# Kernel tuning notes

Hardware: AMD Instinct MI355X
Metric: run time of the kernel (lower is better)

## Reference

```python
import jax, jax.numpy as jnp
import numpy as np

H = 8
D_MODEL = 1024
D_K = D_MODEL // H
NEG = -1000000000.0


def layer_norm(x, a, b, eps=1e-06):
    # torch std: unbiased (ddof=1); module divides by (std + eps)
    mean = jnp.mean(x, axis=-1, keepdims=True)
    var = jnp.sum((x - mean) ** 2, axis=-1, keepdims=True) / (x.shape[-1] - 1)
    std = jnp.sqrt(var)
    return a * (x - mean) / (std + eps) + b


def setup_inputs() -> dict:
    key = jax.random.key(0)
    ks = jax.random.split(key, 12)
    B, S, D = 8, 1024, D_MODEL
    inp = {
        "query": jax.random.normal(ks[0], (B, S, D), jnp.float32),
        "value": jax.random.normal(ks[1], (B, S, D), jnp.float32),
        "key": jax.random.normal(ks[2], (B, S, D), jnp.float32),
        "mask": jax.random.randint(ks[3], (B, S), 0, 2, jnp.int32),
        "ln_a": jnp.ones((D,), jnp.float32),
        "ln_b": jnp.zeros((D,), jnp.float32),
        "wq": jax.random.normal(ks[4], (D, D), jnp.float32) * 0.02,
        "bq": jnp.zeros((D,), jnp.float32),
        "wk": jax.random.normal(ks[5], (D, D), jnp.float32) * 0.02,
        "bk": jnp.zeros((D,), jnp.float32),
        "wv": jax.random.normal(ks[6], (D, D), jnp.float32) * 0.02,
        "bv": jnp.zeros((D,), jnp.float32),
        "w_aoa": jax.random.normal(ks[7], (2 * D, 2 * D), jnp.float32) * 0.02,  # [out, in]
        "b_aoa": jnp.zeros((2 * D,), jnp.float32),
    }
    return inp


def reference(query, value, key, mask, ln_a, ln_b, wq, bq, wk, bk, wv, bv, w_aoa, b_aoa):
    B, S, D = query.shape
    # mask [B,S] -> [B,1,1,S]
    m = mask[:, None, None, :]
    # norm_q
    q = layer_norm(query, ln_a, ln_b)
    # QKV projections, split heads -> [B,H,S,Dk]
    def split_heads(x):
        return x.reshape(B, -1, H, D_K).transpose(0, 2, 1, 3)
    q_ = split_heads(q @ wq.T + bq)
    k_ = split_heads(key @ wk.T + bk)
    v_ = split_heads(value @ wv.T + bv)
    scores = jnp.einsum("bhqd,bhkd->bhqk", q_, k_) / jnp.sqrt(jnp.float32(D_K))
    scores = jnp.where(m == 0, NEG, scores)
    p = jax.nn.softmax(scores, axis=-1)
    x = jnp.einsum("bhqk,bhkd->bhqd", p, v_)
    x = x.transpose(0, 2, 1, 3).reshape(B, S, D)
    # AoA: concat with (normed) query, linear to 2D, GLU
    z = jnp.concatenate([x, q], axis=-1) @ w_aoa.T + b_aoa
    a, g = jnp.split(z, 2, axis=-1)
    return a * jax.nn.sigmoid(g)
```

## Files before the change

kernel.cpp:

```cpp
#include <hip/hip_runtime.h>

typedef __attribute__((ext_vector_type(8))) __bf16 bf16x8;
typedef __attribute__((ext_vector_type(4))) float f32x4;

__device__ __forceinline__ ushort f2b(float f) {
    uint u = __builtin_bit_cast(uint, f);
    u += 0x7fffu + ((u >> 16) & 1u);
    return (ushort)(u >> 16);
}
__device__ __forceinline__ float b2f(ushort h) {
    uint u = ((uint)h) << 16;
    return __builtin_bit_cast(float, u);
}

__global__ __launch_bounds__(256) void cast_kernel(const float* __restrict__ src,
                                                   ushort* __restrict__ dst) {
    size_t i = ((size_t)blockIdx.x * 256 + threadIdx.x) * 4;
    float4 v = *(const float4*)(src + i);
    ushort4 o;
    o.x = f2b(v.x); o.y = f2b(v.y); o.z = f2b(v.z); o.w = f2b(v.w);
    *(ushort4*)(dst + i) = o;
}

__global__ __launch_bounds__(256) void cast_permute_aoa(const float* __restrict__ src,
                                                        ushort* __restrict__ dst) {
    int n1 = blockIdx.x >> 1;
    int c = (blockIdx.x & 1) * 1024 + threadIdx.x * 4;
    int q = ((n1 & 63) | ((n1 >> 7) << 6)) + ((n1 >> 6) & 1) * 1024;
    float4 v = *(const float4*)(src + (size_t)q * 2048 + c);
    ushort4 o;
    o.x = f2b(v.x); o.y = f2b(v.y); o.z = f2b(v.z); o.w = f2b(v.w);
    *(ushort4*)(dst + (size_t)n1 * 2048 + c) = o;
}

__global__ __launch_bounds__(256) void ln_kernel(const float* __restrict__ x,
                                                 const float* __restrict__ ga,
                                                 const float* __restrict__ be,
                                                 ushort* __restrict__ xq) {
    const int row = blockIdx.x, tid = threadIdx.x;
    __shared__ float red[4];
    float4 v = ((const float4*)(x + (size_t)row * 1024))[tid];
    float sm = v.x + v.y + v.z + v.w;
    for (int off = 32; off; off >>= 1) sm += __shfl_xor(sm, off);
    if ((tid & 63) == 0) red[tid >> 6] = sm;
    __syncthreads();
    float mean = (red[0] + red[1] + red[2] + red[3]) * (1.f / 1024.f);
    __syncthreads();
    float dx = v.x - mean, dy = v.y - mean, dz = v.z - mean, dw = v.w - mean;
    float s2 = dx * dx + dy * dy + dz * dz + dw * dw;
    for (int off = 32; off; off >>= 1) s2 += __shfl_xor(s2, off);
    if ((tid & 63) == 0) red[tid >> 6] = s2;
    __syncthreads();
    float var = (red[0] + red[1] + red[2] + red[3]) * (1.f / 1023.f);
    float inv = 1.f / (sqrtf(var) + 1e-6f);
    float4 g = ((const float4*)ga)[tid];
    float4 bb = ((const float4*)be)[tid];
    ushort4 o;
    o.x = f2b(g.x * dx * inv + bb.x);
    o.y = f2b(g.y * dy * inv + bb.y);
    o.z = f2b(g.z * dz * inv + bb.z);
    o.w = f2b(g.w * dw * inv + bb.w);
    *(ushort4*)&xq[(size_t)row * 2048 + 1024 + tid * 4] = o;
}

template <int MODE>
__global__ __launch_bounds__(512, 2) void gemm5(const ushort* __restrict__ Aq, int ldaq,
                                                const ushort* __restrict__ Ak,
                                                const ushort* __restrict__ Av,
                                                const ushort* __restrict__ B, int ldb,
                                                const float* __restrict__ bias0,
                                                const float* __restrict__ bias1,
                                                const float* __restrict__ bias2,
                                                void* __restrict__ out0,
                                                void* __restrict__ out1,
                                                void* __restrict__ out2,
                                                int K, int NB, float qscale) {
    __shared__ ushort lds[2][32768];

    const int tid = threadIdx.x;
    const int w = tid >> 6, l = tid & 63;
    const int wr = w >> 2, wcn = w & 3;
    const int r16 = l & 15, g4 = l >> 4;

    const int bid = blockIdx.x;
    const int cpx = gridDim.x >> 3;
    const int swz = (bid & 7) * cpx + (bid >> 3);
    const int m0 = (swz / NB) * 256;
    const int n0 = (swz % NB) * 256;

    const int region = (MODE == 0) ? (n0 >> 10) : 0;
    const ushort* A = (MODE == 0) ? (region == 0 ? Aq : (region == 1 ? Ak : Av)) : Aq;
    const int lda = (MODE == 0) ? (region == 0 ? ldaq : 1024) : ldaq;

    const int srow8 = l >> 3;
    const int sxor8 = ((l & 7) ^ srow8) * 8;
    const ushort* As0 = A + (size_t)(m0 + w * 8 + srow8) * lda + sxor8;
    const ushort* Bs0 = B + (size_t)(n0 + w * 8 + srow8) * ldb + sxor8;

    f32x4 acc[8][4];
#pragma unroll
    for (int i = 0; i < 8; i++)
#pragma unroll
        for (int j = 0; j < 4; j++) acc[i][j] = (f32x4){0.f, 0.f, 0.f, 0.f};

    const int sw16 = (r16 & 7) << 4;
    char* ldsb = (char*)&lds[0][0];

#define STAGE_H(sel_, HS_, kt_)                                                            \
    do {                                                                                   \
        const int mat_ = (HS_)&1, half_ = (HS_) >> 1;                                      \
        const ushort* sb_ = mat_ ? Bs0 : As0;                                              \
        const int ld_ = mat_ ? ldb : lda;                                                  \
        _Pragma("unroll") for (int li_ = 0; li_ < 2; li_++) {                              \
            const ushort* src_ = sb_ + (size_t)(half_ * 128 + li_ * 64) * ld_ + (kt_)*64;  \
            int dst_ = (sel_)*65536 + mat_ * 32768 + half_ * 16384 + li_ * 8192 + w * 1024;\
            __builtin_amdgcn_global_load_lds(                                              \
                (const __attribute__((address_space(1))) void*)src_,                       \
                (__attribute__((address_space(3))) void*)(ldsb + dst_), 16, 0, 0);         \
        }                                                                                  \
    } while (0)

    auto LDA4 = [&](bf16x8 (&dst)[4][2], int sel, int half) {
#pragma unroll
        for (int ai = 0; ai < 4; ai++)
#pragma unroll
            for (int ks = 0; ks < 2; ks++)
                dst[ai][ks] = *(const bf16x8*)(ldsb + sel * 65536 + half * 16384 +
                                               (wr * 16 + 32 * ai + r16) * 128 +
                                               ((ks * 64 + g4 * 16) ^ sw16));
    };
    auto LDB2 = [&](bf16x8 (&dst)[2][2], int sel, int half) {
#pragma unroll
        for (int bi = 0; bi < 2; bi++)
#pragma unroll
            for (int ks = 0; ks < 2; ks++)
                dst[bi][ks] = *(const bf16x8*)(ldsb + sel * 65536 + 32768 + half * 16384 +
                                               (wcn * 16 + 64 * bi + r16) * 128 +
                                               ((ks * 64 + g4 * 16) ^ sw16));
    };
    auto MM = [&](bf16x8 (&af)[4][2], bf16x8 (&bf)[2][2], int A0, int B0) {
        __builtin_amdgcn_s_setprio(1);
#pragma unroll
        for (int ks = 0; ks < 2; ks++)
#pragma unroll
            for (int ai = 0; ai < 4; ai++)
#pragma unroll
                for (int bi = 0; bi < 2; bi++)
                    acc[A0 + ai][B0 + bi] = __builtin_amdgcn_mfma_f32_16x16x32_bf16(
                        af[ai][ks], bf[bi][ks], acc[A0 + ai][B0 + bi], 0, 0, 0);
        __builtin_amdgcn_s_setprio(0);
    };

    const int NT = K >> 6;

    STAGE_H(0, 0, 0); STAGE_H(0, 1, 0); STAGE_H(0, 2, 0); STAGE_H(0, 3, 0);
    asm volatile("s_waitcnt vmcnt(0)" ::: "memory");
    __builtin_amdgcn_s_barrier();

    bf16x8 aL[4][2], aH[4][2], bL[2][2], bH[2][2];

    for (int t = 0; t < NT; ++t) {
        const int sel = t & 1;
        const bool pf = (t + 1 < NT);
        LDA4(aL, sel, 0); LDB2(bL, sel, 0);
        if (pf) STAGE_H(sel ^ 1, 0, t + 1);
        __builtin_amdgcn_s_barrier();
        MM(aL, bL, 0, 0);
        asm volatile("s_waitcnt vmcnt(4)" ::: "memory");
        __builtin_amdgcn_s_barrier();
        LDA4(aH, sel, 1);
        if (pf) STAGE_H(sel ^ 1, 1, t + 1);
        __builtin_amdgcn_s_barrier();
        MM(aH, bL, 4, 0);
        asm volatile("s_waitcnt vmcnt(4)" ::: "memory");
        __builtin_amdgcn_s_barrier();
        LDB2(bH, sel, 1);
        if (pf) STAGE_H(sel ^ 1, 2, t + 1);
        __builtin_amdgcn_s_barrier();
        MM(aH, bH, 4, 2);
        asm volatile("s_waitcnt vmcnt(4)" ::: "memory");
        __builtin_amdgcn_s_barrier();
        if (pf) STAGE_H(sel ^ 1, 3, t + 1);
        __builtin_amdgcn_s_barrier();
        MM(aL, bH, 0, 2);
        asm volatile("s_waitcnt vmcnt(4)" ::: "memory");
        __builtin_amdgcn_s_barrier();
    }
#undef STAGE_H

    if (MODE == 1) {
        float* out = (float*)out0;
#pragma unroll
        for (int bp = 0; bp < 2; bp++) {
            int j = (n0 >> 1) + wcn * 16 + 64 * bp + r16;
            float bsa = bias0[j];
            float bsg = bias0[j + 1024];
#pragma unroll
            for (int a_ = 0; a_ < 8; a_++) {
                int mr = m0 + wr * 16 + 32 * a_ + g4 * 4;
#pragma unroll
                for (int r = 0; r < 4; r++) {
                    float av = acc[a_][2 * bp][r] + bsa;
                    float gv = acc[a_][2 * bp + 1][r] + bsg;
                    out[(size_t)(mr + r) * 1024 + j] = av * (1.f / (1.f + __expf(-gv)));
                }
            }
        }
    } else {
        const int nr0 = n0 & 1023;
        const float* bias = region == 0 ? bias0 : (region == 1 ? bias1 : bias2);
        const float scale = region == 0 ? qscale : 1.f;
        if (region < 2) {
            ushort* C = (ushort*)(region == 0 ? out0 : out1);
#pragma unroll
            for (int b_ = 0; b_ < 4; b_++) {
                int n = nr0 + wcn * 16 + 64 * b_ + r16;
                float bs = bias[n];
#pragma unroll
                for (int a_ = 0; a_ < 8; a_++) {
                    int mr = m0 + wr * 16 + 32 * a_ + g4 * 4;
#pragma unroll
                    for (int r = 0; r < 4; r++)
                        C[(size_t)(mr + r) * 1024 + n] = f2b((acc[a_][b_][r] + bs) * scale);
                }
            }
        } else {
            ushort* Vt = (ushort*)out2;
#pragma unroll
            for (int b_ = 0; b_ < 4; b_++) {
                int n = nr0 + wcn * 16 + 64 * b_ + r16;
                float bs = bias[n];
                int h = n >> 7, d = n & 127;
#pragma unroll
                for (int a_ = 0; a_ < 8; a_++) {
                    int mr = m0 + wr * 16 + 32 * a_ + g4 * 4;
                    int bb = mr >> 10, s_ = mr & 1023;
                    ushort4 o;
                    o.x = f2b(acc[a_][b_][0] + bs);
                    o.y = f2b(acc[a_][b_][1] + bs);
                    o.z = f2b(acc[a_][b_][2] + bs);
                    o.w = f2b(acc[a_][b_][3] + bs);
                    *(ushort4*)&Vt[((size_t)(bb * 8 + h) * 128 + d) * 1024 + s_] = o;
                }
            }
        }
    }
}

__global__ __launch_bounds__(512, 4) void attn_kernel(const ushort* __restrict__ Q,
                                                      const ushort* __restrict__ Kt,
                                                      const ushort* __restrict__ Vt,
                                                      const int* __restrict__ mask,
                                                      ushort* __restrict__ xq) {
    __shared__ ushort Ks[2][8192];
    __shared__ ushort Vs[2][8192];
    __shared__ ushort Pl[8][1024];

    const int tid = threadIdx.x;
    const int l = tid & 63, wid = tid >> 6;
    const int r16 = l & 15, g4 = l >> 4;
    const int id = blockIdx.x;
    const int bh = ((id >> 6) << 3) | (id & 7);
    const int qb = (id >> 3) & 7;
    const int b = bh >> 3, h = bh & 7;
    const int q0 = qb * 128 + wid * 16;

    bf16x8 qf[4];
    const ushort* Qrow = Q + (size_t)(b * 1024 + q0 + r16) * 1024 + h * 128 + g4 * 8;
#pragma unroll
    for (int kf = 0; kf < 4; kf++) qf[kf] = *(const bf16x8*)(Qrow + kf * 32);

    const ushort* Kg = Kt + ((size_t)b * 1024) * 1024 + h * 128;
    const ushort* Vg = Vt + (size_t)(b * 8 + h) * 128 * 1024;
    const int* mptr = mask + b * 1024;

    f32x4 xacc[8];
#pragma unroll
    for (int i = 0; i < 8; i++) xacc[i] = (f32x4){0.f, 0.f, 0.f, 0.f};
    float mrow = -INFINITY, lrow = 0.f, sclp = 0.f;

    char* Pme = (char*)&Pl[wid][0];
    const int pswz = (r16 & 7) << 4;

    auto STAGE_K = [&](int sel, int t) {
        const int kv0 = t * 64;
#pragma unroll
        for (int it = 0; it < 2; ++it) {
            int ob = it * 8192 + wid * 1024;
            int o = ob + l * 16;
            int row = o >> 8;
            int sc = (o & 255) ^ ((row & 7) << 4);
            const ushort* src = Kg + (size_t)(kv0 + row) * 1024 + (sc >> 1);
            __builtin_amdgcn_global_load_lds((const __attribute__((address_space(1))) void*)src,
                (__attribute__((address_space(3))) void*)((char*)&Ks[sel][0] + ob), 16, 0, 0);
        }
    };
    auto STAGE_V = [&](int sel, int t) {
        const int kv0 = t * 64;
#pragma unroll
        for (int it = 0; it < 2; ++it) {
            int ob = it * 8192 + wid * 1024;
            int o = ob + l * 16;
            int d = o >> 7;
            int sc = (o & 127) ^ ((d & 7) << 4);
            const ushort* src = Vg + (size_t)d * 1024 + kv0 + (sc >> 1);
            __builtin_amdgcn_global_load_lds((const __attribute__((address_space(1))) void*)src,
                (__attribute__((address_space(3))) void*)((char*)&Vs[sel][0] + ob), 16, 0, 0);
        }
    };

    auto QK = [&](f32x4 (&s)[4], int sel, unsigned long long wt) {
        const char* Kb_ = (const char*)&Ks[sel][0];
#pragma unroll
        for (int cg = 0; cg < 4; cg++) {
            s[cg] = (f32x4){0.f, 0.f, 0.f, 0.f};
            const int rowk = cg * 16 + r16;
            const char* kr = Kb_ + rowk * 256;
            const int sw = (rowk & 7) << 4;
            __builtin_amdgcn_s_setprio(1);
#pragma unroll
            for (int kf = 0; kf < 4; kf++) {
                bf16x8 kfr = *(const bf16x8*)(kr + ((kf * 64 + g4 * 16) ^ sw));
                s[cg] = __builtin_amdgcn_mfma_f32_16x16x32_bf16(kfr, qf[kf], s[cg], 0, 0, 0);
            }
            __builtin_amdgcn_s_setprio(0);
            uint nib = (uint)(wt >> (cg * 16 + g4 * 4)) & 15u;
#pragma unroll
            for (int r = 0; r < 4; r++)
                if (!((nib >> r) & 1u)) s[cg][r] = -1e9f;
        }
    };
    auto PV = [&](int sel) {
        const char* Vb_ = (const char*)&Vs[sel][0];
        bf16x8 pfr[2];
#pragma unroll
        for (int ks = 0; ks < 2; ks++)
            pfr[ks] = *(const bf16x8*)(Pme + r16 * 128 + ((g4 * 16 + ks * 64) ^ pswz));
#pragma unroll
        for (int cg2 = 0; cg2 < 8; cg2++)
#pragma unroll
            for (int r = 0; r < 4; r++) xacc[cg2][r] *= sclp;
        __builtin_amdgcn_s_setprio(1);
#pragma unroll
        for (int ks = 0; ks < 2; ks++) {
#pragma unroll
            for (int cg2 = 0; cg2 < 8; cg2++) {
                const int d = cg2 * 16 + r16;
                bf16x8 vfr = *(const bf16x8*)(Vb_ + d * 128 + ((ks * 64 + g4 * 16) ^ ((d & 7) << 4)));
                xacc[cg2] = __builtin_amdgcn_mfma_f32_16x16x32_bf16(vfr, pfr[ks], xacc[cg2], 0, 0, 0);
            }
        }
        __builtin_amdgcn_s_setprio(0);
    };
    auto SOFTMAX = [&](f32x4 (&s)[4]) {
        float pmax = -INFINITY;
#pragma unroll
        for (int cg = 0; cg < 4; cg++)
#pragma unroll
            for (int r = 0; r < 4; r++) pmax = fmaxf(pmax, s[cg][r]);
        pmax = fmaxf(pmax, __shfl_xor(pmax, 16));
        pmax = fmaxf(pmax, __shfl_xor(pmax, 32));
        float mn = fmaxf(mrow, pmax);
        sclp = __expf(mrow - mn);
        mrow = mn;
        float rsum = 0.f;
#pragma unroll
        for (int cg = 0; cg < 4; cg++)
#pragma unroll
            for (int r = 0; r < 4; r++) {
                float p = __expf(s[cg][r] - mn);
                s[cg][r] = p;
                rsum += p;
            }
        rsum += __shfl_xor(rsum, 16);
        rsum += __shfl_xor(rsum, 32);
        lrow = lrow * sclp + rsum;
#pragma unroll
        for (int cg = 0; cg < 4; cg++) {
            uint lo = ((uint)f2b(s[cg][1]) << 16) | f2b(s[cg][0]);
            uint hi = ((uint)f2b(s[cg][3]) << 16) | f2b(s[cg][2]);
            uint2 pk; pk.x = lo; pk.y = hi;
            *(uint2*)(Pme + r16 * 128 + ((cg * 32 + g4 * 8) ^ pswz)) = pk;
        }
    };

    STAGE_K(0, 0);
    int mv = mptr[l];
    asm volatile("s_waitcnt vmcnt(0)" ::: "memory");
    __syncthreads();
    STAGE_K(1, 1);
    STAGE_V(0, 0);
    unsigned long long wt = __ballot(mv != 0);
    mv = mptr[64 + l];
    {
        f32x4 s0[4];
        QK(s0, 0, wt);
        SOFTMAX(s0);
    }
    int kc = 1, vc = 0;

    for (int u = 1; u < 16; ++u) {
        wt = __ballot(mv != 0);
        asm volatile("s_waitcnt vmcnt(0)" ::: "memory");
        __syncthreads();
        if (u < 15) STAGE_K(kc ^ 1, u + 1);
        STAGE_V(vc ^ 1, u);
        if (u < 15) mv = mptr[(u + 1) * 64 + l];

        f32x4 sn[4];
        QK(sn, kc, wt);
        PV(vc);
        SOFTMAX(sn);

        kc ^= 1; vc ^= 1;
    }

    asm volatile("s_waitcnt vmcnt(0)" ::: "memory");
    __syncthreads();
    PV(vc);

    const float inv = 1.f / lrow;
    const size_t orow = (size_t)(b * 1024 + q0 + r16) * 2048 + h * 128;
#pragma unroll
    for (int cg2 = 0; cg2 < 8; cg2++) {
#pragma unroll
        for (int r = 0; r < 4; r++) {
            xq[orow + cg2 * 16 + g4 * 4 + r] = f2b(xacc[cg2][r] * inv);
        }
    }
}

extern "C" void kernel_launch(void* const* d_in, const int* in_sizes, int n_in,
                              void* d_out, int out_size, void* d_ws, size_t ws_size,
                              hipStream_t stream) {
    const float* query = (const float*)d_in[0];
    const float* value = (const float*)d_in[1];
    const float* key   = (const float*)d_in[2];
    const int*   mask  = (const int*)d_in[3];
    const float* ln_a  = (const float*)d_in[4];
    const float* ln_b  = (const float*)d_in[5];
    const float* wq    = (const float*)d_in[6];
    const float* bq    = (const float*)d_in[7];
    const float* wk    = (const float*)d_in[8];
    const float* bk    = (const float*)d_in[9];
    const float* wv    = (const float*)d_in[10];
    const float* bv    = (const float*)d_in[11];
    const float* waoa  = (const float*)d_in[12];
    const float* baoa  = (const float*)d_in[13];
    float* out = (float*)d_out;

    char* w8 = (char*)d_ws;
    ushort* xq   = (ushort*)(w8);
    ushort* Qb   = (ushort*)(w8 + 33554432);
    ushort* Kb   = (ushort*)(w8 + 50331648);
    ushort* Vt   = (ushort*)(w8 + 67108864);
    ushort* keyb = (ushort*)(w8 + 83886080);
    ushort* valb = (ushort*)(w8 + 100663296);
    ushort* wqb  = (ushort*)(w8 + 117440512);
    ushort* wkb  = (ushort*)(w8 + 119537664);
    ushort* wvb  = (ushort*)(w8 + 121634816);
    ushort* wab  = (ushort*)(w8 + 123731968);

    cast_kernel<<<8192, 256, 0, stream>>>(key, keyb);
    cast_kernel<<<8192, 256, 0, stream>>>(value, valb);
    cast_kernel<<<1024, 256, 0, stream>>>(wq, wqb);
    cast_kernel<<<1024, 256, 0, stream>>>(wk, wkb);
    cast_kernel<<<1024, 256, 0, stream>>>(wv, wvb);
    cast_permute_aoa<<<4096, 256, 0, stream>>>(waoa, wab);
    ln_kernel<<<8192, 256, 0, stream>>>(query, ln_a, ln_b, xq);

    const float qscale = 0.08838834764831845f;

    gemm5<0><<<384, 512, 0, stream>>>(xq + 1024, 2048, keyb, valb,
                                      wqb, 1024, bq, bk, bv,
                                      Qb, Kb, Vt, 1024, 12, qscale);

    attn_kernel<<<512, 512, 0, stream>>>(Qb, Kb, Vt, mask, xq);

    gemm5<1><<<256, 512, 0, stream>>>(xq, 2048, nullptr, nullptr,
                                      wab, 2048, baoa, nullptr, nullptr,
                                      out, nullptr, nullptr, 2048, 8, 1.f);
}
```

Measured before the change: 243.7 us.

## Deepen GEMM global-load prefetch to stage tiles two iterations ahead

Restructures the GEMM main loop so global-to-LDS staging runs further ahead. Most of tile t+1 is issued in the prologue, and within each iteration quarters of tile t+2 are staged into the buffer currently being read. The loop ends with two peeled epilogue iterations that drain outstanding loads using adjusted vmcnt waits. The aim is to hide more global memory latency behind MFMA work. It relies on careful barrier placement to avoid overwriting LDS data still being read, and it assumes NT >= 2.

```diff
diff --git a/kernel.cpp b/kernel.cpp
--- a/kernel.cpp
+++ b/kernel.cpp
@@ -64,7 +64,7 @@
 }
 
 template <int MODE>
-__global__ __launch_bounds__(512, 2) void gemm5(const ushort* __restrict__ Aq, int ldaq,
+__global__ __launch_bounds__(512, 2) void gemm6(const ushort* __restrict__ Aq, int ldaq,
                                                 const ushort* __restrict__ Ak,
                                                 const ushort* __restrict__ Av,
                                                 const ushort* __restrict__ B, int ldb,
@@ -154,37 +154,73 @@
     const int NT = K >> 6;
 
     STAGE_H(0, 0, 0); STAGE_H(0, 1, 0); STAGE_H(0, 2, 0); STAGE_H(0, 3, 0);
-    asm volatile("s_waitcnt vmcnt(0)" ::: "memory");
+    STAGE_H(1, 0, 1); STAGE_H(1, 1, 1); STAGE_H(1, 2, 1);
+    asm volatile("s_waitcnt vmcnt(10)" ::: "memory");
     __builtin_amdgcn_s_barrier();
 
     bf16x8 aL[4][2], aH[4][2], bL[2][2], bH[2][2];
 
-    for (int t = 0; t < NT; ++t) {
+    for (int t = 0; t < NT - 2; ++t) {
         const int sel = t & 1;
-        const bool pf = (t + 1 < NT);
         LDA4(aL, sel, 0); LDB2(bL, sel, 0);
-        if (pf) STAGE_H(sel ^ 1, 0, t + 1);
+        STAGE_H(sel ^ 1, 3, t + 1);
         __builtin_amdgcn_s_barrier();
         MM(aL, bL, 0, 0);
-        asm volatile("s_waitcnt vmcnt(4)" ::: "memory");
+        asm volatile("s_waitcnt vmcnt(10)" ::: "memory");
         __builtin_amdgcn_s_barrier();
         LDA4(aH, sel, 1);
-        if (pf) STAGE_H(sel ^ 1, 1, t + 1);
+        STAGE_H(sel, 0, t + 2);
         __builtin_amdgcn_s_barrier();
         MM(aH, bL, 4, 0);
-        asm volatile("s_waitcnt vmcnt(4)" ::: "memory");
+        asm volatile("s_waitcnt vmcnt(10)" ::: "memory");
         __builtin_amdgcn_s_barrier();
         LDB2(bH, sel, 1);
-        if (pf) STAGE_H(sel ^ 1, 2, t + 1);
+        STAGE_H(sel, 1, t + 2);
         __builtin_amdgcn_s_barrier();
         MM(aH, bH, 4, 2);
-        asm volatile("s_waitcnt vmcnt(4)" ::: "memory");
-        __builtin_amdgcn_s_barrier();
-        if (pf) STAGE_H(sel ^ 1, 3, t + 1);
+        __builtin_amdgcn_s_barrier();
+        STAGE_H(sel, 2, t + 2);
+        __builtin_amdgcn_s_barrier();
+        MM(aL, bH, 0, 2);
+        asm volatile("s_waitcnt vmcnt(10)" ::: "memory");
+        __builtin_amdgcn_s_barrier();
+    }
+    {
+        const int sel = (NT - 2) & 1;
+        LDA4(aL, sel, 0); LDB2(bL, sel, 0);
+        STAGE_H(sel ^ 1, 3, NT - 1);
+        __builtin_amdgcn_s_barrier();
+        MM(aL, bL, 0, 0);
+        asm volatile("s_waitcnt vmcnt(10)" ::: "memory");
+        __builtin_amdgcn_s_barrier();
+        LDA4(aH, sel, 1);
+        __builtin_amdgcn_s_barrier();
+        MM(aH, bL, 4, 0);
+        asm volatile("s_waitcnt vmcnt(8)" ::: "memory");
+        __builtin_amdgcn_s_barrier();
+        LDB2(bH, sel, 1);
+        __builtin_amdgcn_s_barrier();
+        MM(aH, bH, 4, 2);
         __builtin_amdgcn_s_barrier();
         MM(aL, bH, 0, 2);
         asm volatile("s_waitcnt vmcnt(4)" ::: "memory");
         __builtin_amdgcn_s_barrier();
+    }
+    {
+        const int sel = (NT - 1) & 1;
+        LDA4(aL, sel, 0); LDB2(bL, sel, 0);
+        __builtin_amdgcn_s_barrier();
+        MM(aL, bL, 0, 0);
+        asm volatile("s_waitcnt vmcnt(2)" ::: "memory");
+        __builtin_amdgcn_s_barrier();
+        LDA4(aH, sel, 1);
+        __builtin_amdgcn_s_barrier();
+        MM(aH, bL, 4, 0);
+        asm volatile("s_waitcnt vmcnt(0)" ::: "memory");
+        __builtin_amdgcn_s_barrier();
+        LDB2(bH, sel, 1);
+        MM(aH, bH, 4, 2);
+        MM(aL, bH, 0, 2);
     }
 #undef STAGE_H
 
@@ -471,13 +507,13 @@
 
     const float qscale = 0.08838834764831845f;
 
-    gemm5<0><<<384, 512, 0, stream>>>(xq + 1024, 2048, keyb, valb,
+    gemm6<0><<<384, 512, 0, stream>>>(xq + 1024, 2048, keyb, valb,
                                       wqb, 1024, bq, bk, bv,
                                       Qb, Kb, Vt, 1024, 12, qscale);
 
     attn_kernel<<<512, 512, 0, stream>>>(Qb, Kb, Vt, mask, xq);
 
-    gemm5<1><<<256, 512, 0, stream>>>(xq, 2048, nullptr, nullptr,
+    gemm6<1><<<256, 512, 0, stream>>>(xq, 2048, nullptr, nullptr,
                                       wab, 2048, baoa, nullptr, nullptr,
                                       out, nullptr, nullptr, 2048, 8, 1.f);
 }
```

After: 236.3 us. 3.0% less time.
